# Kernel tuning notes

Measured on AMD Instinct MI355X. Metric: run time of the kernel, lower is better.

The kernel has to match this reference:

```python
import jax, jax.numpy as jnp
import numpy as np


def setup_inputs() -> dict:
    key = jax.random.key(0)
    k1, k2, k3, k4, k5 = jax.random.split(key, 5)
    N, M, K = 200000, 50, 4
    T = 1000.0
    ti = jnp.sort(jax.random.uniform(k1, (N,), dtype=jnp.float32) * T)
    mi = jax.random.randint(k2, (N,), 0, M, dtype=jnp.int64)
    mu_at_events = jax.random.uniform(k3, (N,), dtype=jnp.float32) * 0.5 + 0.05
    alpha = jax.random.uniform(k4, (K, M, M), dtype=jnp.float32) * 0.1
    gamma = jax.random.uniform(k5, (K,), dtype=jnp.float32) * 2.0 + 0.5
    return {"ti": ti, "mi": mi, "mu_at_events": mu_at_events, "alpha": alpha, "gamma": gamma}


def _hawkes_logsum(ti, mi, mu_at_events, alpha, gamma):
    # ti: [N] sorted event times; mi: [N] event types in [0, M)
    # alpha: [K, M, M]; gamma: [K]; mu_at_events: [N]
    N = ti.shape[0]
    M = alpha.shape[1]
    # inter-event gaps; dt[0] = 0 so the first event has zero excitation state
    dt = jnp.concatenate([jnp.zeros((1,), ti.dtype), ti[1:] - ti[:-1]])  # [N]
    a = jnp.exp(-gamma[None, :] * dt[:, None])  # [N, K] decay factors
    # one-hot of the PREVIOUS event's type (row 0 is all-zero, matching e_mi)
    prev_onehot = jnp.zeros((N, M), ti.dtype).at[jnp.arange(1, N), mi[:-1]].set(1.0)
    b = a[:, None, :] * prev_onehot[:, :, None]  # [N, M, K]

    # linear recurrence S_i = a_i * S_{i-1} + b_i via associative scan
    # combine((a1,b1),(a2,b2)) = (a1*a2, a2*b1 + b2)
    def combine(x, y):
        a1, b1 = x
        a2, b2 = y
        return (a1 * a2, a2[:, None, :] * b1 + b2)

    _, S = jax.lax.associative_scan(combine, (a, b))  # S: [N, M, K]
    # S[i, m, k] = sum_{j < i, m_j = m} exp(-gamma_k (t_i - t_j))
    alpha_at = alpha[:, mi, :]  # [K, N, M] rows of alpha for each event's type
    lam = mu_at_events + jnp.einsum('knm,nmk,k->n', alpha_at, S, gamma)  # [N]
    return jnp.sum(jnp.log(lam))


def reference(ti, mi, mu_at_events, alpha, gamma):
    return _hawkes_logsum(ti, mi, mu_at_events, alpha, gamma)
```

## Files before the change

kernel.cpp:

```cpp
#include <hip/hip_runtime.h>

#define CHUNK 256
#define MM 50
#define KK 4
#define STATE 200
#define ASTRIDE 51
#define SUP 32
#define NSMAX 26
#define GMAX 1024

__device__ int   g_ticket;
__device__ float g_chunkB[GMAX * STATE];
__device__ float g_superB[64 * STATE];

__device__ __forceinline__ unsigned short f2bf(float x) {
  unsigned u = __float_as_uint(x);
  u += 0x7fffu + ((u >> 16) & 1u);
  return (unsigned short)(u >> 16);
}
__device__ __forceinline__ float bflo(unsigned u) { return __uint_as_float(u << 16); }
__device__ __forceinline__ float bfhi(unsigned u) { return __uint_as_float(u & 0xffff0000u); }

__device__ __forceinline__ void st_agent(float* p, float v) {
  __hip_atomic_store(p, v, __ATOMIC_RELAXED, __HIP_MEMORY_SCOPE_AGENT);
}
__device__ __forceinline__ float ld_agent(const float* p) {
  return __hip_atomic_load(p, __ATOMIC_RELAXED, __HIP_MEMORY_SCOPE_AGENT);
}

__global__ __launch_bounds__(512) void hawkes_df(
    const float* __restrict__ ti, const int* __restrict__ mi,
    const float* __restrict__ mu, const float* __restrict__ alpha,
    const float* __restrict__ gamma, float* __restrict__ out,
    int N, int G, int NB) {
  int tid = threadIdx.x;
  __shared__ int vid_s;
  __shared__ uint2 P[MM * ASTRIDE];
  __shared__ __align__(16) float4 Fj[512];
  __shared__ int   cj[512];
  __shared__ __align__(16) float Q[16][STATE];
  __shared__ float teL[SUP];
  __shared__ float tlast[NSMAX];
  __shared__ float red8[8];

  if (tid == 0) vid_s = atomicAdd(&g_ticket, 1);

  int b = blockIdx.x;
  int c0 = 2 * b;
  int lQ = c0 * CHUNK;
  int sup = b >> 4;
  int g0c = sup * SUP;
  int nloc = c0 - g0c;
  int ch = tid >> 8;

  float gk0 = gamma[0], gk1 = gamma[1], gk2 = gamma[2], gk3 = gamma[3];

  for (int i = tid; i < 16 * STATE; i += 512) ((float*)Q)[i] = 0.f;
  if (tid < SUP) {
    int c = g0c + tid;
    if (c < G) teL[tid] = ti[min(N, (c + 1) * CHUNK) - 1];
  } else if (tid >= 64 && tid < 64 + NSMAX) {
    int s = tid - 64;
    if (s < sup) tlast[s] = ti[min(N, (s + 1) * SUP * CHUNK) - 1];
  }
  if (b == 0 && tid == 0) st_agent(out, 0.f);

  float tref_ch = ti[(b == 0 && ch == 0) ? 0 : (lQ + ch * CHUNK - 1)];
  int n = lQ + tid;
  bool has_n = (n < N);
  float ti_n = has_n ? ti[n] : 0.f;
  int   mi_n = has_n ? mi[n] : 0;
  float mu_n = has_n ? mu[n] : 0.f;
  int j = lQ - 1 + tid;
  float ti_j = __shfl_up(ti_n, 1, 64);
  int   mi_j = __shfl_up(mi_n, 1, 64);
  if ((tid & 63) == 0 && j >= 0) { ti_j = ti[j]; mi_j = mi[j]; }
  bool valid = (j >= 0) && has_n;
  int myc = valid ? mi_j : 0;
  float4 F = make_float4(0.f, 0.f, 0.f, 0.f);
  if (valid) {
    float tj = ti_j - tref_ch;
    F = make_float4(__expf(gk0 * tj), __expf(gk1 * tj),
                    __expf(gk2 * tj), __expf(gk3 * tj));
  }
  cj[tid] = myc;
  Fj[tid] = F;
  __syncthreads();

  if (valid) {
    float* q = &Q[tid >> 5][myc * KK];
    atomicAdd(q + 0, F.x); atomicAdd(q + 1, F.y);
    atomicAdd(q + 2, F.z); atomicAdd(q + 3, F.w);
  }
  #pragma unroll
  for (int u = 0; u < 5; ++u) {
    int idx = tid + 512 * u;
    if (idx < MM * MM) {
      int c = idx / MM, cp = idx - c * MM;
      float a0 = gk0 * alpha[idx];
      float a1 = gk1 * alpha[2500 + idx];
      float a2 = gk2 * alpha[5000 + idx];
      float a3 = gk3 * alpha[7500 + idx];
      P[c * ASTRIDE + cp] =
          make_uint2((unsigned)f2bf(a0) | ((unsigned)f2bf(a1) << 16),
                     (unsigned)f2bf(a2) | ((unsigned)f2bf(a3) << 16));
    }
  }
  __syncthreads();

  float epoch_s = ((vid_s / NB) & 1) ? -1.f : 1.f;
  float gkc = (tid & 2) ? ((tid & 1) ? gk3 : gk2) : ((tid & 1) ? gk1 : gk0);
  float totA = 0.f, totB = 0.f, dA = 0.f, dB = 0.f;
  if (tid < STATE) {
    #pragma unroll
    for (int q = 0; q < 8; ++q)  totA += Q[q][tid];
    #pragma unroll
    for (int q = 8; q < 16; ++q) totB += Q[q][tid];
    dA = __expf(-gkc * (teL[nloc] - tref_ch));
    dB = __expf(-gkc * (teL[nloc + 1] - teL[nloc]));
    st_agent(&g_chunkB[(size_t)c0 * STATE + tid], epoch_s * (dA * totA + 1.f));
    st_agent(&g_chunkB[(size_t)(c0 + 1) * STATE + tid], epoch_s * (dB * totB + 1.f));
  }

  float4 acc = make_float4(0.f, 0.f, 0.f, 0.f);
  if (has_n) {
    int rowb = mi_n * ASTRIDE;
    int base = tid & ~31;
    #pragma unroll 4
    for (int s = base; s <= tid; ++s) {
      uint2 p = P[rowb + cj[s]];
      float4 f = Fj[s];
      acc.x += bflo(p.x) * f.x; acc.y += bfhi(p.x) * f.y;
      acc.z += bflo(p.y) * f.z; acc.w += bfhi(p.y) * f.w;
    }
  }

  bool closer = ((b & 15) == 15) || (b == NB - 1);
  float S = 0.f;
  if (tid < STATE) {
    for (int u0 = 0; u0 < nloc; u0 += 16) {
      float r[16];
      #pragma unroll
      for (int u = 0; u < 16; ++u)
        r[u] = (u0 + u < nloc)
             ? ld_agent(&g_chunkB[(size_t)(g0c + u0 + u) * STATE + tid])
             : epoch_s;
      #pragma unroll
      for (int u = 0; u < 16; ++u) {
        if (u0 + u < nloc) {
          float v = r[u];
          while (epoch_s * v < 0.5f) {
            __builtin_amdgcn_s_sleep(1);
            v = ld_agent(&g_chunkB[(size_t)(g0c + u0 + u) * STATE + tid]);
          }
          S += __expf(-gkc * (tref_ch - teL[u0 + u])) * (epoch_s * v - 1.f);
        }
      }
    }
    if (closer) {
      float run2 = dA * (S + totA);
      run2 = dB * (run2 + totB);
      st_agent(&g_superB[(size_t)sup * STATE + tid], epoch_s * (run2 + 1.f));
    }
    for (int s0 = 0; s0 < sup; s0 += 16) {
      float r[16];
      #pragma unroll
      for (int u = 0; u < 16; ++u)
        r[u] = (s0 + u < sup)
             ? ld_agent(&g_superB[(size_t)(s0 + u) * STATE + tid])
             : epoch_s;
      #pragma unroll
      for (int u = 0; u < 16; ++u) {
        if (s0 + u < sup) {
          float v = r[u];
          while (epoch_s * v < 0.5f) {
            __builtin_amdgcn_s_sleep(1);
            v = ld_agent(&g_superB[(size_t)(s0 + u) * STATE + tid]);
          }
          S += __expf(-gkc * (tref_ch - tlast[s0 + u])) * (epoch_s * v - 1.f);
        }
      }
    }
    float run = S;
    #pragma unroll
    for (int q = 0; q < 8; ++q)  { float t = Q[q][tid]; Q[q][tid] = run; run += t; }
    run = dA * run;
    #pragma unroll
    for (int q = 8; q < 16; ++q) { float t = Q[q][tid]; Q[q][tid] = run; run += t; }
  }
  __syncthreads();

  float local = 0.f;
  if (has_n) {
    int rowb = mi_n * ASTRIDE;
    const float4* wb = (const float4*)&Q[tid >> 5][0];
    #pragma unroll 10
    for (int m = 0; m < MM; ++m) {
      uint2 p = P[rowb + m];
      float4 w = wb[m];
      acc.x += bflo(p.x) * w.x; acc.y += bfhi(p.x) * w.y;
      acc.z += bflo(p.y) * w.z; acc.w += bfhi(p.y) * w.w;
    }
    float tn = ti_n - tref_ch;
    float lam = mu_n
              + __expf(-gk0 * tn) * acc.x + __expf(-gk1 * tn) * acc.y
              + __expf(-gk2 * tn) * acc.z + __expf(-gk3 * tn) * acc.w;
    local = __logf(lam);
  }
  #pragma unroll
  for (int off = 32; off > 0; off >>= 1)
    local += __shfl_down(local, off, 64);
  if ((tid & 63) == 0) red8[tid >> 6] = local;
  __syncthreads();
  if (tid == 0) {
    float acc8 = 0.f;
    #pragma unroll
    for (int w = 0; w < 8; ++w) acc8 += red8[w];
    atomicAdd(out, acc8);
  }
}

extern "C" void kernel_launch(void* const* d_in, const int* in_sizes, int n_in,
                              void* d_out, int out_size, void* d_ws, size_t ws_size,
                              hipStream_t stream) {
  const float* ti    = (const float*)d_in[0];
  const int*   mi    = (const int*)d_in[1];
  const float* mu    = (const float*)d_in[2];
  const float* alpha = (const float*)d_in[3];
  const float* gamma = (const float*)d_in[4];
  float* out = (float*)d_out;
  int N = in_sizes[0];
  int G = (N + CHUNK - 1) / CHUNK;
  if (G > GMAX) return;
  int NB = (G + 1) / 2;

  hawkes_df<<<NB, 512, 0, stream>>>(ti, mi, mu, alpha, gamma, out, N, G, NB);
}
```

Baseline: 86.39 us.

## Split cross-block prefix lookback across two thread groups and split alpha table

The decoupled lookback that sums earlier chunk and superchunk states is now split between two 200-thread groups (even and odd entries), which halves the serial spin-wait chain per thread. The partial sums are combined through shared memory, with an extra barrier for closer blocks. The packed alpha table is also split from uint2 into two separate 32-bit shared arrays, likely to avoid 64-bit LDS bank conflicts given the odd stride. The second chunk's reference time is now loaded directly and the lookback uses a single reference time. The cost is extra shared memory and barriers.

```diff
diff --git a/kernel.cpp b/kernel.cpp
--- a/kernel.cpp
+++ b/kernel.cpp
@@ -35,10 +35,13 @@
     int N, int G, int NB) {
   int tid = threadIdx.x;
   __shared__ int vid_s;
-  __shared__ uint2 P[MM * ASTRIDE];
+  __shared__ unsigned P0[MM * ASTRIDE];
+  __shared__ unsigned P1[MM * ASTRIDE];
   __shared__ __align__(16) float4 Fj[512];
   __shared__ int   cj[512];
   __shared__ __align__(16) float Q[16][STATE];
+  __shared__ float SB1[STATE];
+  __shared__ float SB2[STATE];
   __shared__ float teL[SUP];
   __shared__ float tlast[NSMAX];
   __shared__ float red8[8];
@@ -65,7 +68,8 @@
   }
   if (b == 0 && tid == 0) st_agent(out, 0.f);
 
-  float tref_ch = ti[(b == 0 && ch == 0) ? 0 : (lQ + ch * CHUNK - 1)];
+  float tref0 = ti[(b == 0) ? 0 : (lQ - 1)];
+  float tref_ch = ch ? ti[min(N - 1, lQ + CHUNK - 1)] : tref0;
   int n = lQ + tid;
   bool has_n = (n < N);
   float ti_n = has_n ? ti[n] : 0.f;
@@ -101,9 +105,8 @@
       float a1 = gk1 * alpha[2500 + idx];
       float a2 = gk2 * alpha[5000 + idx];
       float a3 = gk3 * alpha[7500 + idx];
-      P[c * ASTRIDE + cp] =
-          make_uint2((unsigned)f2bf(a0) | ((unsigned)f2bf(a1) << 16),
-                     (unsigned)f2bf(a2) | ((unsigned)f2bf(a3) << 16));
+      P0[c * ASTRIDE + cp] = (unsigned)f2bf(a0) | ((unsigned)f2bf(a1) << 16);
+      P1[c * ASTRIDE + cp] = (unsigned)f2bf(a2) | ((unsigned)f2bf(a3) << 16);
     }
   }
   __syncthreads();
@@ -116,7 +119,7 @@
     for (int q = 0; q < 8; ++q)  totA += Q[q][tid];
     #pragma unroll
     for (int q = 8; q < 16; ++q) totB += Q[q][tid];
-    dA = __expf(-gkc * (teL[nloc] - tref_ch));
+    dA = __expf(-gkc * (teL[nloc] - tref0));
     dB = __expf(-gkc * (teL[nloc + 1] - teL[nloc]));
     st_agent(&g_chunkB[(size_t)c0 * STATE + tid], epoch_s * (dA * totA + 1.f));
     st_agent(&g_chunkB[(size_t)(c0 + 1) * STATE + tid], epoch_s * (dB * totB + 1.f));
@@ -128,65 +131,112 @@
     int base = tid & ~31;
     #pragma unroll 4
     for (int s = base; s <= tid; ++s) {
-      uint2 p = P[rowb + cj[s]];
+      unsigned p0 = P0[rowb + cj[s]];
+      unsigned p1 = P1[rowb + cj[s]];
       float4 f = Fj[s];
-      acc.x += bflo(p.x) * f.x; acc.y += bfhi(p.x) * f.y;
-      acc.z += bflo(p.y) * f.z; acc.w += bfhi(p.y) * f.w;
+      acc.x += bflo(p0) * f.x; acc.y += bfhi(p0) * f.y;
+      acc.z += bflo(p1) * f.z; acc.w += bfhi(p1) * f.w;
     }
   }
 
   bool closer = ((b & 15) == 15) || (b == NB - 1);
-  float S = 0.f;
-  if (tid < STATE) {
-    for (int u0 = 0; u0 < nloc; u0 += 16) {
-      float r[16];
-      #pragma unroll
-      for (int u = 0; u < 16; ++u)
-        r[u] = (u0 + u < nloc)
-             ? ld_agent(&g_chunkB[(size_t)(g0c + u0 + u) * STATE + tid])
-             : epoch_s;
-      #pragma unroll
-      for (int u = 0; u < 16; ++u) {
-        if (u0 + u < nloc) {
-          float v = r[u];
-          while (epoch_s * v < 0.5f) {
-            __builtin_amdgcn_s_sleep(1);
-            v = ld_agent(&g_chunkB[(size_t)(g0c + u0 + u) * STATE + tid]);
-          }
-          S += __expf(-gkc * (tref_ch - teL[u0 + u])) * (epoch_s * v - 1.f);
+  bool grpA = (tid < STATE);
+  bool grpB = (tid >= 256) && (tid < 256 + STATE);
+  int st = grpB ? (tid - 256) : tid;
+  float SA = 0.f;
+
+  int cpar = nloc >> 1;
+  if (grpA && cpar) {
+    float r[15];
+    #pragma unroll
+    for (int i = 0; i < 15; ++i)
+      r[i] = (i < cpar) ? ld_agent(&g_chunkB[(size_t)(g0c + 2 * i) * STATE + st]) : epoch_s;
+    #pragma unroll
+    for (int i = 0; i < 15; ++i) if (i < cpar) {
+      float v = r[i];
+      while (epoch_s * v < 0.5f) {
+        __builtin_amdgcn_s_sleep(1);
+        v = ld_agent(&g_chunkB[(size_t)(g0c + 2 * i) * STATE + st]);
+      }
+      SA += __expf(-gkc * (tref0 - teL[2 * i])) * (epoch_s * v - 1.f);
+    }
+  }
+  if (grpB) {
+    float PB = 0.f;
+    if (cpar) {
+      float r[15];
+      #pragma unroll
+      for (int i = 0; i < 15; ++i)
+        r[i] = (i < cpar) ? ld_agent(&g_chunkB[(size_t)(g0c + 2 * i + 1) * STATE + st]) : epoch_s;
+      #pragma unroll
+      for (int i = 0; i < 15; ++i) if (i < cpar) {
+        float v = r[i];
+        while (epoch_s * v < 0.5f) {
+          __builtin_amdgcn_s_sleep(1);
+          v = ld_agent(&g_chunkB[(size_t)(g0c + 2 * i + 1) * STATE + st]);
         }
-      }
-    }
-    if (closer) {
-      float run2 = dA * (S + totA);
+        PB += __expf(-gkc * (tref0 - teL[2 * i + 1])) * (epoch_s * v - 1.f);
+      }
+    }
+    SB1[st] = PB;
+  }
+
+  if (closer) {
+    __syncthreads();
+    if (grpA) {
+      float Sin = SA + SB1[st];
+      float run2 = dA * (Sin + totA);
       run2 = dB * (run2 + totB);
-      st_agent(&g_superB[(size_t)sup * STATE + tid], epoch_s * (run2 + 1.f));
-    }
-    for (int s0 = 0; s0 < sup; s0 += 16) {
-      float r[16];
-      #pragma unroll
-      for (int u = 0; u < 16; ++u)
-        r[u] = (s0 + u < sup)
-             ? ld_agent(&g_superB[(size_t)(s0 + u) * STATE + tid])
-             : epoch_s;
-      #pragma unroll
-      for (int u = 0; u < 16; ++u) {
-        if (s0 + u < sup) {
-          float v = r[u];
-          while (epoch_s * v < 0.5f) {
-            __builtin_amdgcn_s_sleep(1);
-            v = ld_agent(&g_superB[(size_t)(s0 + u) * STATE + tid]);
-          }
-          S += __expf(-gkc * (tref_ch - tlast[s0 + u])) * (epoch_s * v - 1.f);
+      st_agent(&g_superB[(size_t)sup * STATE + st], epoch_s * (run2 + 1.f));
+      SA = Sin;
+    }
+  }
+
+  int cse = (sup + 1) >> 1, cso = sup >> 1;
+  if (grpA && cse) {
+    float r[13];
+    #pragma unroll
+    for (int i = 0; i < 13; ++i)
+      r[i] = (i < cse) ? ld_agent(&g_superB[(size_t)(2 * i) * STATE + st]) : epoch_s;
+    #pragma unroll
+    for (int i = 0; i < 13; ++i) if (i < cse) {
+      float v = r[i];
+      while (epoch_s * v < 0.5f) {
+        __builtin_amdgcn_s_sleep(1);
+        v = ld_agent(&g_superB[(size_t)(2 * i) * STATE + st]);
+      }
+      SA += __expf(-gkc * (tref0 - tlast[2 * i])) * (epoch_s * v - 1.f);
+    }
+  }
+  if (grpB) {
+    float PB2 = 0.f;
+    if (cso) {
+      float r[12];
+      #pragma unroll
+      for (int i = 0; i < 12; ++i)
+        r[i] = (i < cso) ? ld_agent(&g_superB[(size_t)(2 * i + 1) * STATE + st]) : epoch_s;
+      #pragma unroll
+      for (int i = 0; i < 12; ++i) if (i < cso) {
+        float v = r[i];
+        while (epoch_s * v < 0.5f) {
+          __builtin_amdgcn_s_sleep(1);
+          v = ld_agent(&g_superB[(size_t)(2 * i + 1) * STATE + st]);
         }
-      }
-    }
+        PB2 += __expf(-gkc * (tref0 - tlast[2 * i + 1])) * (epoch_s * v - 1.f);
+      }
+    }
+    SB2[st] = PB2;
+  }
+  __syncthreads();
+
+  if (grpA) {
+    float S = SA + SB2[st] + (closer ? 0.f : SB1[st]);
     float run = S;
     #pragma unroll
-    for (int q = 0; q < 8; ++q)  { float t = Q[q][tid]; Q[q][tid] = run; run += t; }
+    for (int q = 0; q < 8; ++q)  { float t = Q[q][st]; Q[q][st] = run; run += t; }
     run = dA * run;
     #pragma unroll
-    for (int q = 8; q < 16; ++q) { float t = Q[q][tid]; Q[q][tid] = run; run += t; }
+    for (int q = 8; q < 16; ++q) { float t = Q[q][st]; Q[q][st] = run; run += t; }
   }
   __syncthreads();
 
@@ -196,10 +246,11 @@
     const float4* wb = (const float4*)&Q[tid >> 5][0];
     #pragma unroll 10
     for (int m = 0; m < MM; ++m) {
-      uint2 p = P[rowb + m];
+      unsigned p0 = P0[rowb + m];
+      unsigned p1 = P1[rowb + m];
       float4 w = wb[m];
-      acc.x += bflo(p.x) * w.x; acc.y += bfhi(p.x) * w.y;
-      acc.z += bflo(p.y) * w.z; acc.w += bfhi(p.y) * w.w;
+      acc.x += bflo(p0) * w.x; acc.y += bfhi(p0) * w.y;
+      acc.z += bflo(p1) * w.z; acc.w += bfhi(p1) * w.w;
     }
     float tn = ti_n - tref_ch;
     float lam = mu_n
```

Measured after the change: 85.86 us. Within noise of the previous version (-0.6%).
